# Kernel optimization log

Measured on AMD Instinct MI355X. Metric: run time of the kernel, lower is better.

The kernel has to match this reference:

```python
import jax, jax.numpy as jnp
import numpy as np

OUT_H, OUT_W = 7, 7
SPATIAL_SCALE = 0.25
SAMPLING_RATIO = 2  # fixed sampling grid per bin (sampling_ratio > 0 branch)


def setup_inputs() -> dict:
    key = jax.random.key(0)
    k1, k2, k3, k4, k5 = jax.random.split(key, 5)
    B, C, H, W = 2, 256, 200, 200
    N = 1000
    features = jax.random.normal(k1, (B, C, H, W), dtype=jnp.float32)
    # rois: [batch_idx, cx, cy, w, h, theta] in IMAGE coords (image = 800x800 since scale=0.25)
    batch_idx = jax.random.randint(k2, (N,), 0, B).astype(jnp.float32)
    centers = jax.random.uniform(k3, (N, 2), minval=100.0, maxval=700.0)
    sizes = jax.random.uniform(k4, (N, 2), minval=32.0, maxval=256.0)
    angles = jax.random.uniform(k5, (N, 1), minval=0.0, maxval=float(np.pi))
    rois = jnp.concatenate([batch_idx[:, None], centers, sizes, angles], axis=1).astype(jnp.float32)
    return {"features": features, "rois": rois}


def _roi_align_rotated(features, rois, out_h, out_w, scale, g):
    B, C, H, W = features.shape
    N = rois.shape[0]
    b = rois[:, 0].astype(jnp.int32)
    cx = rois[:, 1] * scale
    cy = rois[:, 2] * scale
    rw = jnp.maximum(rois[:, 3] * scale, 1.0)
    rh = jnp.maximum(rois[:, 4] * scale, 1.0)
    theta = rois[:, 5]
    bin_h = rh / out_h
    bin_w = rw / out_w
    # sample offsets within the roi: yy = -h/2 + (s + 0.5) * bin/g for s in [0, out*g)
    sy = (jnp.arange(out_h * g, dtype=features.dtype) + 0.5) / g  # [Hs] in bin units
    sx = (jnp.arange(out_w * g, dtype=features.dtype) + 0.5) / g  # [Ws]
    yy = -rh[:, None] * 0.5 + sy[None, :] * bin_h[:, None]  # [N, Hs]
    xx = -rw[:, None] * 0.5 + sx[None, :] * bin_w[:, None]  # [N, Ws]
    cos_t = jnp.cos(theta)[:, None, None]
    sin_t = jnp.sin(theta)[:, None, None]
    # rotate around roi center (mmcv / detectron2 convention)
    y = yy[:, :, None] * cos_t - xx[:, None, :] * sin_t + cy[:, None, None]  # [N, Hs, Ws]
    x = yy[:, :, None] * sin_t + xx[:, None, :] * cos_t + cx[:, None, None]
    # bilinear_interpolate semantics from the CUDA kernel
    inside = (y >= -1.0) & (y <= H) & (x >= -1.0) & (x <= W)
    yc = jnp.clip(y, 0.0)
    xc = jnp.clip(x, 0.0)
    yl = jnp.minimum(jnp.floor(yc).astype(jnp.int32), H - 1)
    xl = jnp.minimum(jnp.floor(xc).astype(jnp.int32), W - 1)
    yh = jnp.minimum(yl + 1, H - 1)
    xh = jnp.minimum(xl + 1, W - 1)
    ly = jnp.where(jnp.floor(yc) >= H - 1, 0.0, yc - yl)
    lx = jnp.where(jnp.floor(xc) >= W - 1, 0.0, xc - xl)
    hy = 1.0 - ly
    hx = 1.0 - lx
    bi = b[:, None, None]
    v1 = features[bi, :, yl, xl]  # [N, Hs, Ws, C]
    v2 = features[bi, :, yl, xh]
    v3 = features[bi, :, yh, xl]
    v4 = features[bi, :, yh, xh]
    w1 = (hy * hx)[..., None]
    w2 = (hy * lx)[..., None]
    w3 = (ly * hx)[..., None]
    w4 = (ly * lx)[..., None]
    val = w1 * v1 + w2 * v2 + w3 * v3 + w4 * v4
    val = jnp.where(inside[..., None], val, 0.0)
    # average over the g x g samples per output bin
    val = val.reshape(N, out_h, g, out_w, g, C).mean(axis=(2, 4))  # [N, out_h, out_w, C]
    return jnp.transpose(val, (0, 3, 1, 2))  # [N, C, out_h, out_w]


def reference(features, rois):
    return _roi_align_rotated(features, rois, OUT_H, OUT_W, SPATIAL_SCALE, SAMPLING_RATIO)
```

## Files before the change

kernel.cpp:

```cpp
#include <hip/hip_runtime.h>
#include <hip/hip_fp16.h>


#define B_ 2
#define C_ 256
#define H_ 200
#define W_ 200
#define OUTHW 7
#define GRID_S 14
#define NSAMP 196
#define ELEMS (C_ * OUTHW * OUTHW)

__global__ __launch_bounds__(256) void transpose_h_kernel(
    const float* __restrict__ feat, __half* __restrict__ featT)
{
    __shared__ float tile[64][65];
    const int x0   = blockIdx.x * 64;
    const int c0   = blockIdx.y * 64;
    const int yb   = blockIdx.z;
    const int y    = yb % H_;
    const int b    = yb / H_;
    const int t    = threadIdx.x;
    const int lane = t & 63;
    const int grp  = t >> 6;
    const int nx   = min(64, W_ - x0);

    if (lane < nx) {
        #pragma unroll
        for (int i = 0; i < 16; ++i) {
            const int cl = grp * 16 + i;
            tile[cl][lane] =
                feat[((size_t)(b * C_ + c0 + cl) * H_ + y) * W_ + x0 + lane];
        }
    }
    __syncthreads();

    const int c = (t & 7) * 8;
    #pragma unroll
    for (int pass = 0; pass < 2; ++pass) {
        const int p = pass * 32 + (t >> 3);
        if (p < nx) {
            union { __half h[8]; uint4 u; } pk;
            #pragma unroll
            for (int k = 0; k < 8; ++k)
                pk.h[k] = __float2half(tile[c + k][p]);
            *reinterpret_cast<uint4*>(
                &featT[((size_t)(b * H_ + y) * W_ + x0 + p) * C_ + c0 + c]) = pk.u;
        }
    }
}

__device__ __forceinline__ void build_table(
    const float* __restrict__ rois, int n, int t,
    float s_w[4][NSAMP], int s_idx[4][NSAMP], int pix_stride, int fold_batch,
    int* s_b)
{
    const float spatial_scale = 0.25f;
    if (t == 0 && s_b) *s_b = (int)rois[n * 6 + 0];
    if (t < NSAMP) {
        const int   b  = (int)rois[n * 6 + 0];
        const float cx = rois[n * 6 + 1] * spatial_scale;
        const float cy = rois[n * 6 + 2] * spatial_scale;
        const float rw = fmaxf(rois[n * 6 + 3] * spatial_scale, 1.0f);
        const float rh = fmaxf(rois[n * 6 + 4] * spatial_scale, 1.0f);
        const float th = rois[n * 6 + 5];
        const float cosv = cosf(th), sinv = sinf(th);

        const float bin_h = rh * (1.0f / OUTHW);
        const float bin_w = rw * (1.0f / OUTHW);
        const int row = t / GRID_S;
        const int col = t % GRID_S;

        const float yy = -rh * 0.5f + ((float)row + 0.5f) * 0.5f * bin_h;
        const float xx = -rw * 0.5f + ((float)col + 0.5f) * 0.5f * bin_w;

        const float y = yy * cosv - xx * sinv + cy;
        const float x = yy * sinv + xx * cosv + cx;

        const bool inside = (y >= -1.0f) && (y <= (float)H_) &&
                            (x >= -1.0f) && (x <= (float)W_);

        const float yc = fmaxf(y, 0.0f);
        const float xc = fmaxf(x, 0.0f);
        const float fy = floorf(yc);
        const float fx = floorf(xc);
        int yl = min((int)fy, H_ - 1);
        int xl = min((int)fx, W_ - 1);
        const int yh = min(yl + 1, H_ - 1);
        const int xh = min(xl + 1, W_ - 1);
        const float ly = (fy >= (float)(H_ - 1)) ? 0.0f : (yc - fy);
        const float lx = (fx >= (float)(W_ - 1)) ? 0.0f : (xc - fx);
        const float hy = 1.0f - ly;
        const float hx = 1.0f - lx;

        const float m = inside ? 0.25f : 0.0f;
        s_w[0][t] = hy * hx * m;
        s_w[1][t] = hy * lx * m;
        s_w[2][t] = ly * hx * m;
        s_w[3][t] = ly * lx * m;
        const int bb = fold_batch ? b : 0;
        s_idx[0][t] = ((bb * H_ + yl) * W_ + xl) * pix_stride;
        s_idx[1][t] = ((bb * H_ + yl) * W_ + xh) * pix_stride;
        s_idx[2][t] = ((bb * H_ + yh) * W_ + xl) * pix_stride;
        s_idx[3][t] = ((bb * H_ + yh) * W_ + xh) * pix_stride;
    }
}

__global__ __launch_bounds__(256) void roi_main_nhwc_h(
    const __half* __restrict__ featT,
    const float* __restrict__ rois,
    float* __restrict__ out)
{
    __shared__ float  s_w[4][NSAMP];
    __shared__ int    s_idx[4][NSAMP];
    __shared__ __half s_out[49][258];

    const int n = blockIdx.x;
    const int t = threadIdx.x;
    build_table(rois, n, t, s_w, s_idx, C_, 1, nullptr);
    __syncthreads();

    const int lane  = t & 63;
    const int wave  = t >> 6;
    const int cbase = lane * 4;

    for (int bl = wave; bl < OUTHW * OUTHW; bl += 4) {
        const int oy = bl / OUTHW;
        const int ox = bl - oy * OUTHW;

        int   off[16];
        float w[16];
        #pragma unroll
        for (int j = 0; j < 2; ++j) {
            #pragma unroll
            for (int i = 0; i < 2; ++i) {
                const int s = (oy * 2 + j) * GRID_S + (ox * 2 + i);
                #pragma unroll
                for (int q = 0; q < 4; ++q) {
                    const int k = (j * 2 + i) * 4 + q;
                    w[k]   = s_w[q][s];
                    off[k] = s_idx[q][s] + cbase;
                }
            }
        }

        uint2 r[16];
        #pragma unroll
        for (int k = 0; k < 16; ++k)
            r[k] = *reinterpret_cast<const uint2*>(featT + off[k]);

        __builtin_amdgcn_sched_barrier(0);

        float a0 = 0.f, a1 = 0.f, a2 = 0.f, a3 = 0.f;
        #pragma unroll
        for (int k = 0; k < 16; ++k) {
            const __half2* h2 = reinterpret_cast<const __half2*>(&r[k]);
            const float2 f0 = __half22float2(h2[0]);
            const float2 f1 = __half22float2(h2[1]);
            a0 += w[k] * f0.x; a1 += w[k] * f0.y;
            a2 += w[k] * f1.x; a3 += w[k] * f1.y;
        }

        s_out[bl][0 * 64 + lane] = __float2half(a0);
        s_out[bl][1 * 64 + lane] = __float2half(a1);
        s_out[bl][2 * 64 + lane] = __float2half(a2);
        s_out[bl][3 * 64 + lane] = __float2half(a3);
    }
    __syncthreads();

    float* __restrict__ ob = out + (size_t)n * ELEMS;
    for (int k = 0; k < 49; ++k) {
        const int e   = t + k * 256;
        const int c   = e / 49;
        const int bin = e - c * 49;
        __builtin_nontemporal_store(
            __half2float(s_out[bin][(c & 3) * 64 + (c >> 2)]), &ob[e]);
    }
}

__global__ __launch_bounds__(256) void roi_main_nchw(
    const float* __restrict__ feat,
    const float* __restrict__ rois,
    float* __restrict__ out)
{
    const int n = blockIdx.x;
    const int t = threadIdx.x;
    __shared__ float s_w[4][NSAMP];
    __shared__ int   s_idx[4][NSAMP];
    __shared__ int   s_b;

    build_table(rois, n, t, s_w, s_idx, 1, 0, &s_b);
    __syncthreads();

    const float* __restrict__ fb = feat + (size_t)s_b * (size_t)(C_ * H_ * W_);
    float* __restrict__ ob = out + (size_t)n * (size_t)ELEMS;

    for (int e = t; e < ELEMS; e += 256) {
        const int c   = e / 49;
        const int bin = e - c * 49;
        const int oy  = bin / 7;
        const int ox  = bin - oy * 7;
        const float* __restrict__ fc = fb + c * (H_ * W_);
        float acc = 0.0f;
        #pragma unroll
        for (int j = 0; j < 2; ++j) {
            #pragma unroll
            for (int i = 0; i < 2; ++i) {
                const int s = (oy * 2 + j) * GRID_S + (ox * 2 + i);
                acc += s_w[0][s] * fc[s_idx[0][s]];
                acc += s_w[1][s] * fc[s_idx[1][s]];
                acc += s_w[2][s] * fc[s_idx[2][s]];
                acc += s_w[3][s] * fc[s_idx[3][s]];
            }
        }
        ob[e] = acc;
    }
}

extern "C" void kernel_launch(void* const* d_in, const int* in_sizes, int n_in,
                              void* d_out, int out_size, void* d_ws, size_t ws_size,
                              hipStream_t stream) {
    const float* feat = (const float*)d_in[0];
    const float* rois = (const float*)d_in[1];
    float* out = (float*)d_out;
    const int N = in_sizes[1] / 6;

    const size_t need = (size_t)B_ * H_ * W_ * C_ * sizeof(__half);
    if (ws_size >= need) {
        __half* featT = (__half*)d_ws;
        dim3 tg((W_ + 63) / 64, C_ / 64, H_ * B_);
        transpose_h_kernel<<<tg, 256, 0, stream>>>(feat, featT);
        roi_main_nhwc_h<<<N, 256, 0, stream>>>(featT, rois, out);
    } else {
        roi_main_nchw<<<N, 256, 0, stream>>>(feat, rois, out);
    }
}
```

Measured before the change: 183.8 us.

## Sort ROIs by batch and y-center and map blocks per XCD for L2 locality

Block (0,0,0) of the transpose kernel now computes a permutation of ROIs, sorted by batch index and then center y with an O(N^2) rank sort in shared memory. The main kernel assigns each contiguous chunk of the sorted list to blocks that share the same blockIdx mod 8, which on MI355X's eight XCDs should keep spatially nearby ROIs on one XCD and improve L2 reuse of the feature map. The cost is extra serial sort work inside one transpose block, which may lengthen that kernel's tail, plus a perm lookup in every main-kernel block. It also relies on blocks being dispatched round-robin across XCDs.

```diff
diff --git a/kernel.cpp b/kernel.cpp
--- a/kernel.cpp
+++ b/kernel.cpp
@@ -10,11 +10,14 @@
 #define GRID_S 14
 #define NSAMP 196
 #define ELEMS (C_ * OUTHW * OUTHW)
+#define FEATT_BYTES ((size_t)B_ * H_ * W_ * C_ * sizeof(__half))
 
 __global__ __launch_bounds__(256) void transpose_h_kernel(
-    const float* __restrict__ feat, __half* __restrict__ featT)
+    const float* __restrict__ feat, __half* __restrict__ featT,
+    const float* __restrict__ rois, int* __restrict__ perm, int N)
 {
     __shared__ float tile[64][65];
+    __shared__ float s_key[1024];
     const int x0   = blockIdx.x * 64;
     const int c0   = blockIdx.y * 64;
     const int yb   = blockIdx.z;
@@ -46,6 +49,25 @@
                 pk.h[k] = __float2half(tile[c + k][p]);
             *reinterpret_cast<uint4*>(
                 &featT[((size_t)(b * H_ + y) * W_ + x0 + p) * C_ + c0 + c]) = pk.u;
+        }
+    }
+
+    if (blockIdx.x == 0 && blockIdx.y == 0 && blockIdx.z == 0) {
+        if (N <= 1024) {
+            for (int i = t; i < N; i += 256)
+                s_key[i] = rois[i * 6 + 0] * 10000.0f + rois[i * 6 + 2];
+            __syncthreads();
+            for (int i = t; i < N; i += 256) {
+                const float ki = s_key[i];
+                int r = 0;
+                for (int j = 0; j < N; ++j) {
+                    const float kj = s_key[j];
+                    r += (int)((kj < ki) | ((kj == ki) & (j < i)));
+                }
+                perm[r] = i;
+            }
+        } else {
+            for (int i = t; i < N; i += 256) perm[i] = i;
         }
     }
 }
@@ -109,13 +131,21 @@
 __global__ __launch_bounds__(256) void roi_main_nhwc_h(
     const __half* __restrict__ featT,
     const float* __restrict__ rois,
+    const int* __restrict__ perm, int N,
     float* __restrict__ out)
 {
     __shared__ float  s_w[4][NSAMP];
     __shared__ int    s_idx[4][NSAMP];
     __shared__ __half s_out[49][258];
 
-    const int n = blockIdx.x;
+    const int k = blockIdx.x & 7;
+    const int j = blockIdx.x >> 3;
+    const int q = N >> 3, rem = N & 7;
+    const int sz = q + (k < rem ? 1 : 0);
+    if (j >= sz) return;
+    const int r = (k < rem ? k * (q + 1) : rem * (q + 1) + (k - rem) * q) + j;
+    const int n = perm[r];
+
     const int t = threadIdx.x;
     build_table(rois, n, t, s_w, s_idx, C_, 1, nullptr);
     __syncthreads();
@@ -131,34 +161,34 @@
         int   off[16];
         float w[16];
         #pragma unroll
-        for (int j = 0; j < 2; ++j) {
+        for (int jj = 0; jj < 2; ++jj) {
             #pragma unroll
             for (int i = 0; i < 2; ++i) {
-                const int s = (oy * 2 + j) * GRID_S + (ox * 2 + i);
+                const int s = (oy * 2 + jj) * GRID_S + (ox * 2 + i);
                 #pragma unroll
-                for (int q = 0; q < 4; ++q) {
-                    const int k = (j * 2 + i) * 4 + q;
-                    w[k]   = s_w[q][s];
-                    off[k] = s_idx[q][s] + cbase;
+                for (int qq = 0; qq < 4; ++qq) {
+                    const int kk = (jj * 2 + i) * 4 + qq;
+                    w[kk]   = s_w[qq][s];
+                    off[kk] = s_idx[qq][s] + cbase;
                 }
             }
         }
 
-        uint2 r[16];
-        #pragma unroll
-        for (int k = 0; k < 16; ++k)
-            r[k] = *reinterpret_cast<const uint2*>(featT + off[k]);
+        uint2 rv[16];
+        #pragma unroll
+        for (int kk = 0; kk < 16; ++kk)
+            rv[kk] = *reinterpret_cast<const uint2*>(featT + off[kk]);
 
         __builtin_amdgcn_sched_barrier(0);
 
         float a0 = 0.f, a1 = 0.f, a2 = 0.f, a3 = 0.f;
         #pragma unroll
-        for (int k = 0; k < 16; ++k) {
-            const __half2* h2 = reinterpret_cast<const __half2*>(&r[k]);
+        for (int kk = 0; kk < 16; ++kk) {
+            const __half2* h2 = reinterpret_cast<const __half2*>(&rv[kk]);
             const float2 f0 = __half22float2(h2[0]);
             const float2 f1 = __half22float2(h2[1]);
-            a0 += w[k] * f0.x; a1 += w[k] * f0.y;
-            a2 += w[k] * f1.x; a3 += w[k] * f1.y;
+            a0 += w[kk] * f0.x; a1 += w[kk] * f0.y;
+            a2 += w[kk] * f1.x; a3 += w[kk] * f1.y;
         }
 
         s_out[bl][0 * 64 + lane] = __float2half(a0);
@@ -169,8 +199,8 @@
     __syncthreads();
 
     float* __restrict__ ob = out + (size_t)n * ELEMS;
-    for (int k = 0; k < 49; ++k) {
-        const int e   = t + k * 256;
+    for (int kk = 0; kk < 49; ++kk) {
+        const int e   = t + kk * 256;
         const int c   = e / 49;
         const int bin = e - c * 49;
         __builtin_nontemporal_store(
@@ -225,12 +255,15 @@
     float* out = (float*)d_out;
     const int N = in_sizes[1] / 6;
 
-    const size_t need = (size_t)B_ * H_ * W_ * C_ * sizeof(__half);
-    if (ws_size >= need) {
+    const size_t perm_bytes = (size_t)((N + 7) & ~7) * sizeof(int);
+    const size_t need = FEATT_BYTES + perm_bytes;
+    if (ws_size >= need && N >= 8) {
         __half* featT = (__half*)d_ws;
+        int* perm = (int*)((char*)d_ws + FEATT_BYTES);
         dim3 tg((W_ + 63) / 64, C_ / 64, H_ * B_);
-        transpose_h_kernel<<<tg, 256, 0, stream>>>(feat, featT);
-        roi_main_nhwc_h<<<N, 256, 0, stream>>>(featT, rois, out);
+        transpose_h_kernel<<<tg, 256, 0, stream>>>(feat, featT, rois, perm, N);
+        const int nblk = 8 * ((N + 7) / 8);
+        roi_main_nhwc_h<<<nblk, 256, 0, stream>>>(featT, rois, perm, N, out);
     } else {
         roi_main_nchw<<<N, 256, 0, stream>>>(feat, rois, out);
     }
```

Measured after the change: 241.3 us. 1.31x slower.
